# Performance work log

Measured on AMD Instinct MI355X. Metric: run time of the kernel, lower is better.

## Reference

```python
import jax, jax.numpy as jnp
import numpy as np

HID, H, D, DFF = 128, 4, 128, 2048   # hidden_dim, nheads, out_feats per head, dim_feedforward
N, E, B = 32768, 524288, 32
EPS = 1e-5
SLOPE = 0.2  # DGL EdgeGATConv negative_slope default


def setup_inputs() -> dict:
    key = jax.random.key(0)
    ks = jax.random.split(key, 16)
    s = 0.05
    return {
        "h": jax.random.normal(ks[0], (N, HID), jnp.float32),
        "e": jax.random.normal(ks[1], (E, 1), jnp.float32),
        "src": jax.random.randint(ks[2], (E,), 0, N, jnp.int32),
        "dst": jax.random.randint(ks[3], (E,), 0, N, jnp.int32),
        "batch_size": B,
        # EdgeGATConv params (fc / fc_edge / res_fc are bias-free in DGL)
        "W_fc": jax.random.normal(ks[4], (HID, H * D), jnp.float32) * s,
        "attn_l": jax.random.normal(ks[5], (H, D), jnp.float32) * s,
        "attn_r": jax.random.normal(ks[6], (H, D), jnp.float32) * s,
        "W_fe": jax.random.normal(ks[7], (1, H * D), jnp.float32) * s,
        "attn_e": jax.random.normal(ks[8], (H, D), jnp.float32) * s,
        "W_res": jax.random.normal(ks[9], (HID, H * D), jnp.float32) * s,
        "gat_bias": jnp.zeros((H * D,), jnp.float32),
        # linear_mha + norms + FFN
        "W_mha": jax.random.normal(ks[10], (H * D, HID), jnp.float32) * s,
        "b_mha": jnp.zeros((HID,), jnp.float32),
        "n1_g": jnp.ones((HID,), jnp.float32),
        "n1_b": jnp.zeros((HID,), jnp.float32),
        "n2_g": jnp.ones((HID,), jnp.float32),
        "n2_b": jnp.zeros((HID,), jnp.float32),
        "W1": jax.random.normal(ks[11], (HID, DFF), jnp.float32) * s,
        "b1": jnp.zeros((DFF,), jnp.float32),
        "W2": jax.random.normal(ks[12], (DFF, HID), jnp.float32) * s,
        "b2": jnp.zeros((HID,), jnp.float32),
    }


def _ln(x, g, b):
    mu = x.mean(-1, keepdims=True)
    var = ((x - mu) ** 2).mean(-1, keepdims=True)
    return (x - mu) * jax.lax.rsqrt(var + EPS) * g + b


def reference(h, e, src, dst, batch_size, W_fc, attn_l, attn_r, W_fe, attn_e,
              W_res, gat_bias, W_mha, b_mha, n1_g, n1_b, n2_g, n2_b,
              W1, b1, W2, b2):
    n = h.shape[0]
    h0 = h
    # --- EdgeGATConv (eval mode: dropouts are identity) ---
    ft = (h @ W_fc).reshape(n, H, D)                         # (N,H,D)
    el = jnp.einsum("nhd,hd->nh", ft, attn_l)                # (N,H)
    er = jnp.einsum("nhd,hd->nh", ft, attn_r)
    fe = (e @ W_fe).reshape(-1, H, D)                        # (E,H,D)
    ee = jnp.einsum("ehd,hd->eh", fe, attn_e)                # (E,H)
    sc = jax.nn.leaky_relu(el[src] + er[dst] + ee, SLOPE)    # (E,H)
    # segment softmax over incoming edges of each dst node
    m = jax.ops.segment_max(sc, dst, num_segments=n)         # (N,H)
    m = jnp.where(jnp.isfinite(m), m, 0.0)                   # empty segments
    w = jnp.exp(sc - m[dst])
    z = jax.ops.segment_sum(w, dst, num_segments=n)
    zd = z[dst]
    alpha = w / jnp.where(zd == 0, 1.0, zd)                  # (E,H)
    msg = ft[src] * alpha[:, :, None]                        # (E,H,D)
    rst = jax.ops.segment_sum(msg, dst, num_segments=n)      # (N,H,D)
    rst = rst + (h0 @ W_res).reshape(n, H, D) + gat_bias.reshape(1, H, D)
    # --- transformer wrapper ---
    x = jax.nn.relu(rst).reshape(n, H * D)
    x = jax.nn.relu(x @ W_mha + b_mha)
    x = _ln(h0 + x, n1_g, n1_b)
    x = x.reshape(batch_size, -1, x.shape[1])                # (B, N/B, HID)
    ff = jax.nn.relu(x @ W1 + b1) @ W2 + b2
    return _ln(x + ff, n2_g, n2_b)
```

## Files before the change

### kernel.cpp

```cpp
#include <hip/hip_runtime.h>
#include <hip/hip_bf16.h>

#define N_NODES 32768
#define E_EDGES 524288
#define HIDDIM 128
#define FDIM 512
#define DFF 2048
#define LN_EPS 1e-5f
#define SLOPE 0.2f
#define CAP 64

typedef __bf16 bf16_t;
typedef __bf16 bf16x8 __attribute__((ext_vector_type(8)));
typedef float f32x4 __attribute__((ext_vector_type(4)));
typedef float f32x2 __attribute__((ext_vector_type(2)));

#define GLD_LDS16(gp, lp) __builtin_amdgcn_global_load_lds( \
    (const __attribute__((address_space(1))) unsigned int*)(gp), \
    (__attribute__((address_space(3))) unsigned int*)(lp), 16, 0, 0)

__device__ inline unsigned char f32_to_e4m3(float v) {
#if __has_builtin(__builtin_amdgcn_cvt_pk_fp8_f32)
    return (unsigned char)(__builtin_amdgcn_cvt_pk_fp8_f32(v, v, 0, false) & 0xff);
#else
    unsigned bits = __float_as_uint(v);
    unsigned sign = (bits >> 24) & 0x80;
    float av = fabsf(v);
    if (av >= 448.f) return (unsigned char)(sign | 0x7E);
    int e = (int)((bits >> 23) & 0xFF) - 127;
    if (e < -6) { int n = (int)rintf(av * 512.f); return (unsigned char)(sign | n); }
    float ulp = exp2f((float)(e - 3));
    int n = (int)rintf(av / ulp);
    if (n == 16) { e += 1; n = 8; }
    return (unsigned char)(sign | ((e + 7) << 3) | (n - 8));
#endif
}
template<bool HI>
__device__ inline f32x2 e4m3x2_to_f32(unsigned u) {
#if __has_builtin(__builtin_amdgcn_cvt_pk_f32_fp8)
    return __builtin_amdgcn_cvt_pk_f32_fp8(u, HI);
#else
    f32x2 r;
    unsigned b0 = HI ? ((u >> 16) & 0xff) : (u & 0xff);
    unsigned b1 = HI ? ((u >> 24) & 0xff) : ((u >> 8) & 0xff);
    unsigned bs[2] = {b0, b1};
    for (int i = 0; i < 2; ++i) {
        unsigned b = bs[i];
        float s = (b & 0x80) ? -1.f : 1.f;
        int e = (b >> 3) & 15, m = b & 7;
        float v = e ? (8 + m) * exp2f((float)(e - 10)) : m * exp2f(-9.f);
        r[i] = s * v;
    }
    return r;
#endif
}

__device__ inline void pack_range(const float* __restrict__ B, bf16_t* __restrict__ out,
                                  int id, int N) {
    const int g = id / N, n = id % N;
    union { bf16_t b[8]; uint4 u; } pk;
#pragma unroll
    for (int j = 0; j < 8; ++j) pk.b[j] = (bf16_t)B[(size_t)(g * 8 + j) * N + n];
    *(uint4*)(out + (size_t)id * 8) = pk.u;
}

__global__ __launch_bounds__(256) void prep_kernel(const float* __restrict__ h, bf16_t* __restrict__ hb,
                                                   const float* __restrict__ W_fc, bf16_t* __restrict__ Wfc_p,
                                                   const float* __restrict__ W_res, bf16_t* __restrict__ Wres_p,
                                                   const float* __restrict__ W_mha, bf16_t* __restrict__ Wmha_p,
                                                   const float* __restrict__ W1, bf16_t* __restrict__ W1_p,
                                                   const float* __restrict__ W2, bf16_t* __restrict__ W2_p,
                                                   const float* __restrict__ W_fe, const float* __restrict__ attn_e,
                                                   float* __restrict__ ce) {
    int bid = blockIdx.x;
    const int tid = threadIdx.x;
    if (bid < 4096) {
        const int id = bid * 256 + tid;
        const float4 v = ((const float4*)h)[id];
        union { bf16_t b[4]; uint2 u; } pk;
        pk.b[0] = (bf16_t)v.x; pk.b[1] = (bf16_t)v.y; pk.b[2] = (bf16_t)v.z; pk.b[3] = (bf16_t)v.w;
        *(uint2*)(hb + (size_t)id * 4) = pk.u;
        return;
    }
    bid -= 4096;
    if (bid < 32)  { pack_range(W_fc,  Wfc_p,  bid * 256 + tid, 512);  return; }
    bid -= 32;
    if (bid < 32)  { pack_range(W_res, Wres_p, bid * 256 + tid, 512);  return; }
    bid -= 32;
    if (bid < 32)  { pack_range(W_mha, Wmha_p, bid * 256 + tid, 128);  return; }
    bid -= 32;
    if (bid < 128) { pack_range(W1,    W1_p,   bid * 256 + tid, 2048); return; }
    bid -= 128;
    if (bid < 128) { pack_range(W2,    W2_p,   bid * 256 + tid, 128);  return; }
    if (tid < 128) {
        const float4 w = ((const float4*)W_fe)[tid];
        const float4 a = ((const float4*)attn_e)[tid];
        float p = w.x * a.x + w.y * a.y + w.z * a.z + w.w * a.w;
        for (int off = 16; off; off >>= 1) p += __shfl_down(p, off, 32);
        if ((tid & 31) == 0) ce[tid >> 5] = p;
    }
}

__global__ __launch_bounds__(256) void gemm_mfma(const bf16_t* __restrict__ A,
                                                 const bf16_t* __restrict__ Bp,
                                                 bf16_t* __restrict__ C,
                                                 int M, int N, int K) {
    __shared__ __align__(16) bf16_t lA[4096];
    __shared__ __align__(16) bf16_t lB[4096];
    const int tid = threadIdx.x;
    const int lane = tid & 63;
    const int wave = tid >> 6;
    const int wm = (wave >> 1) * 64, wn = (wave & 1) * 64;
    const int row0 = blockIdx.y * 128, col0 = blockIdx.x * 128;
    const int ko = lane >> 4;
    const int rl = lane & 15;
    f32x4 acc[4][4] = {};
    const int c0 = tid, c1 = tid + 256;
    const int g0 = c0 >> 7, m0 = c0 & 127;
    const int g1 = c1 >> 7, m1 = c1 & 127;
    for (int k0 = 0; k0 < K; k0 += 32) {
        __syncthreads();
        GLD_LDS16(A + (size_t)(row0 + m0) * K + k0 + g0 * 8, lA + c0 * 8);
        GLD_LDS16(A + (size_t)(row0 + m1) * K + k0 + g1 * 8, lA + c1 * 8);
        GLD_LDS16(Bp + ((size_t)(k0 / 8 + g0) * N + col0 + m0) * 8, lB + c0 * 8);
        GLD_LDS16(Bp + ((size_t)(k0 / 8 + g1) * N + col0 + m1) * 8, lB + c1 * 8);
        __syncthreads();
        bf16x8 af[4], bfr[4];
#pragma unroll
        for (int i = 0; i < 4; ++i) {
            af[i]  = *(const bf16x8*)&lA[(ko * 128 + wm + i * 16 + rl) * 8];
            bfr[i] = *(const bf16x8*)&lB[(ko * 128 + wn + i * 16 + rl) * 8];
        }
#pragma unroll
        for (int i = 0; i < 4; ++i)
#pragma unroll
            for (int j = 0; j < 4; ++j)
                acc[i][j] = __builtin_amdgcn_mfma_f32_16x16x32_bf16(af[i], bfr[j], acc[i][j], 0, 0, 0);
    }
    const int cr = (lane >> 4) * 4;
    const int cc = lane & 15;
#pragma unroll
    for (int i = 0; i < 4; ++i)
#pragma unroll
        for (int j = 0; j < 4; ++j) {
            const int col = col0 + wn + j * 16 + cc;
#pragma unroll
            for (int r = 0; r < 4; ++r) {
                const int row = row0 + wm + i * 16 + cr + r;
                C[(size_t)row * N + col] = (bf16_t)acc[i][j][r];
            }
        }
}

__global__ __launch_bounds__(256) void gemm_ft(const bf16_t* __restrict__ A,
                                               const bf16_t* __restrict__ Bp,
                                               const float* __restrict__ attn_l,
                                               const float* __restrict__ attn_r,
                                               unsigned char* __restrict__ ft8,
                                               float* __restrict__ el,
                                               float* __restrict__ er) {
    __shared__ __align__(16) bf16_t lA[4096];
    __shared__ __align__(16) bf16_t lB[4096];
    __shared__ float s_el[2][128], s_er[2][128];
    const int tid = threadIdx.x, lane = tid & 63, wave = tid >> 6;
    const int wm = (wave >> 1) * 64, wn = (wave & 1) * 64;
    const int row0 = blockIdx.y * 128;
    const int head = blockIdx.x, col0 = head * 128;
    const int ko = lane >> 4, rl = lane & 15;
    f32x4 acc[4][4] = {};
    const int c0 = tid, c1 = tid + 256;
    const int g0 = c0 >> 7, m0 = c0 & 127;
    const int g1 = c1 >> 7, m1 = c1 & 127;
    for (int k0 = 0; k0 < 128; k0 += 32) {
        __syncthreads();
        GLD_LDS16(A + (size_t)(row0 + m0) * 128 + k0 + g0 * 8, lA + c0 * 8);
        GLD_LDS16(A + (size_t)(row0 + m1) * 128 + k0 + g1 * 8, lA + c1 * 8);
        GLD_LDS16(Bp + ((size_t)(k0 / 8 + g0) * 512 + col0 + m0) * 8, lB + c0 * 8);
        GLD_LDS16(Bp + ((size_t)(k0 / 8 + g1) * 512 + col0 + m1) * 8, lB + c1 * 8);
        __syncthreads();
        bf16x8 af[4], bfr[4];
#pragma unroll
        for (int i = 0; i < 4; ++i) {
            af[i]  = *(const bf16x8*)&lA[(ko * 128 + wm + i * 16 + rl) * 8];
            bfr[i] = *(const bf16x8*)&lB[(ko * 128 + wn + i * 16 + rl) * 8];
        }
#pragma unroll
        for (int i = 0; i < 4; ++i)
#pragma unroll
            for (int j = 0; j < 4; ++j)
                acc[i][j] = __builtin_amdgcn_mfma_f32_16x16x32_bf16(af[i], bfr[j], acc[i][j], 0, 0, 0);
    }
    const int cr = (lane >> 4) * 4, cc = lane & 15;
    float al[4], ar[4];
#pragma unroll
    for (int j = 0; j < 4; ++j) {
        al[j] = attn_l[col0 + wn + j * 16 + cc];
        ar[j] = attn_r[col0 + wn + j * 16 + cc];
    }
#pragma unroll
    for (int i = 0; i < 4; ++i)
#pragma unroll
        for (int r = 0; r < 4; ++r) {
            const int row = row0 + wm + i * 16 + cr + r;
            float pel = 0.f, per = 0.f;
#pragma unroll
            for (int j = 0; j < 4; ++j) {
                const float v = acc[i][j][r];
                ft8[(size_t)row * 512 + col0 + wn + j * 16 + cc] = f32_to_e4m3(v);
                pel += v * al[j];
                per += v * ar[j];
            }
#pragma unroll
            for (int m = 1; m < 16; m <<= 1) {
                pel += __shfl_xor(pel, m);
                per += __shfl_xor(per, m);
            }
            if (cc == 0) {
                s_el[wn >> 6][wm + i * 16 + cr + r] = pel;
                s_er[wn >> 6][wm + i * 16 + cr + r] = per;
            }
        }
    __syncthreads();
    if (tid < 128) {
        el[(size_t)(row0 + tid) * 4 + head] = s_el[0][tid] + s_el[1][tid];
        er[(size_t)(row0 + tid) * 4 + head] = s_er[0][tid] + s_er[1][tid];
    }
}

__global__ __launch_bounds__(256) void gemm_mha_ln(const bf16_t* __restrict__ A,
                                                   const bf16_t* __restrict__ Bp,
                                                   const float* __restrict__ bias,
                                                   const float* __restrict__ h0,
                                                   const float* __restrict__ gamma,
                                                   const float* __restrict__ beta,
                                                   bf16_t* __restrict__ out) {
    __shared__ __align__(16) bf16_t lA[4096];
    __shared__ __align__(16) bf16_t lB[4096];
    __shared__ float s_s1[2][128], s_s2[2][128], s_mu[128], s_rs[128];
    const int tid = threadIdx.x, lane = tid & 63, wave = tid >> 6;
    const int wm = (wave >> 1) * 64, wn = (wave & 1) * 64;
    const int row0 = blockIdx.x * 128;
    const int ko = lane >> 4, rl = lane & 15;
    f32x4 acc[4][4] = {};
    const int c0 = tid, c1 = tid + 256;
    const int g0 = c0 >> 7, m0 = c0 & 127;
    const int g1 = c1 >> 7, m1 = c1 & 127;
    for (int k0 = 0; k0 < 512; k0 += 32) {
        __syncthreads();
        GLD_LDS16(A + (size_t)(row0 + m0) * 512 + k0 + g0 * 8, lA + c0 * 8);
        GLD_LDS16(A + (size_t)(row0 + m1) * 512 + k0 + g1 * 8, lA + c1 * 8);
        GLD_LDS16(Bp + ((size_t)(k0 / 8 + g0) * 128 + m0) * 8, lB + c0 * 8);
        GLD_LDS16(Bp + ((size_t)(k0 / 8 + g1) * 128 + m1) * 8, lB + c1 * 8);
        __syncthreads();
        bf16x8 af[4], bfr[4];
#pragma unroll
        for (int i = 0; i < 4; ++i) {
            af[i]  = *(const bf16x8*)&lA[(ko * 128 + wm + i * 16 + rl) * 8];
            bfr[i] = *(const bf16x8*)&lB[(ko * 128 + wn + i * 16 + rl) * 8];
        }
#pragma unroll
        for (int i = 0; i < 4; ++i)
#pragma unroll
            for (int j = 0; j < 4; ++j)
                acc[i][j] = __builtin_amdgcn_mfma_f32_16x16x32_bf16(af[i], bfr[j], acc[i][j], 0, 0, 0);
    }
    const int cr = (lane >> 4) * 4, cc = lane & 15;
#pragma unroll
    for (int j = 0; j < 4; ++j) {
        const int col = wn + j * 16 + cc;
        const float bb = bias[col];
#pragma unroll
        for (int i = 0; i < 4; ++i)
#pragma unroll
            for (int r = 0; r < 4; ++r) {
                const int row = row0 + wm + i * 16 + cr + r;
                acc[i][j][r] = fmaxf(acc[i][j][r] + bb, 0.f) + h0[(size_t)row * 128 + col];
            }
    }
#pragma unroll
    for (int i = 0; i < 4; ++i)
#pragma unroll
        for (int r = 0; r < 4; ++r) {
            float s1 = 0.f, s2 = 0.f;
#pragma unroll
            for (int j = 0; j < 4; ++j) { const float v = acc[i][j][r]; s1 += v; s2 += v * v; }
#pragma unroll
            for (int m = 1; m < 16; m <<= 1) {
                s1 += __shfl_xor(s1, m);
                s2 += __shfl_xor(s2, m);
            }
            if (cc == 0) {
                s_s1[wn >> 6][wm + i * 16 + cr + r] = s1;
                s_s2[wn >> 6][wm + i * 16 + cr + r] = s2;
            }
        }
    __syncthreads();
    if (tid < 128) {
        const float a = s_s1[0][tid] + s_s1[1][tid];
        const float q = s_s2[0][tid] + s_s2[1][tid];
        const float mu = a * (1.f / 128.f);
        s_mu[tid] = mu;
        s_rs[tid] = rsqrtf(q * (1.f / 128.f) - mu * mu + LN_EPS);
    }
    __syncthreads();
#pragma unroll
    for (int j = 0; j < 4; ++j) {
        const int col = wn + j * 16 + cc;
        const float gg = gamma[col], bb = beta[col];
#pragma unroll
        for (int i = 0; i < 4; ++i)
#pragma unroll
            for (int r = 0; r < 4; ++r) {
                const int rloc = wm + i * 16 + cr + r;
                out[(size_t)(row0 + rloc) * 128 + col] =
                    (bf16_t)((acc[i][j][r] - s_mu[rloc]) * s_rs[rloc] * gg + bb);
            }
    }
}

__global__ __launch_bounds__(256, 2) void ffn_fused(const bf16_t* __restrict__ x3,
                                                    const bf16_t* __restrict__ W1p,
                                                    const float* __restrict__ b1,
                                                    const bf16_t* __restrict__ W2p,
                                                    const float* __restrict__ b2,
                                                    const float* __restrict__ gamma,
                                                    const float* __restrict__ beta,
                                                    float* __restrict__ out) {
    __shared__ __align__(16) bf16_t lW1[8192];
    __shared__ __align__(16) bf16_t lW2[8192];
    __shared__ __align__(16) bf16_t lY[4096];
    __shared__ float s_s1[2][64], s_s2[2][64], s_mu[64], s_rs[64];
    const int tid = threadIdx.x, lane = tid & 63, wave = tid >> 6;
    const int wr  = (wave >> 1) * 32;
    const int wc1 = (wave & 1) * 32;
    const int wc2 = (wave & 1) * 64;
    const int row0 = blockIdx.x * 64;
    const int ko = lane >> 4, rl = lane & 15;
    const int cr = ko * 4, cc = rl;

#pragma unroll
    for (int it = 0; it < 4; ++it) {
        const int c = it * 256 + tid, g = c >> 6, m = c & 63;
        GLD_LDS16(x3 + (size_t)(row0 + m) * 128 + g * 8, lW1 + c * 8);
    }
    __syncthreads();
    bf16x8 afx[2][4];
#pragma unroll
    for (int i = 0; i < 2; ++i)
#pragma unroll
        for (int kk = 0; kk < 4; ++kk)
            afx[i][kk] = *(const bf16x8*)&lW1[((kk * 4 + ko) * 64 + wr + i * 16 + rl) * 8];

    f32x4 xacc[2][4] = {};
    for (int ch = 0; ch < 32; ++ch) {
        __syncthreads();
#pragma unroll
        for (int it = 0; it < 4; ++it) {
            const int c = it * 256 + tid;
            { const int g = c >> 6, n = c & 63;  GLD_LDS16(W1p + ((size_t)g * 2048 + ch * 64 + n) * 8, lW1 + c * 8); }
            { const int g = c >> 7, n = c & 127; GLD_LDS16(W2p + ((size_t)(ch * 8 + g) * 128 + n) * 8, lW2 + c * 8); }
        }
        __syncthreads();
        f32x4 yacc[2][2] = {};
#pragma unroll
        for (int kk = 0; kk < 4; ++kk) {
            bf16x8 bfr[2];
#pragma unroll
            for (int j = 0; j < 2; ++j)
                bfr[j] = *(const bf16x8*)&lW1[((kk * 4 + ko) * 64 + wc1 + j * 16 + rl) * 8];
#pragma unroll
            for (int i = 0; i < 2; ++i)
#pragma unroll
                for (int j = 0; j < 2; ++j)
                    yacc[i][j] = __builtin_amdgcn_mfma_f32_16x16x32_bf16(afx[i][kk], bfr[j], yacc[i][j], 0, 0, 0);
        }
#pragma unroll
        for (int j = 0; j < 2; ++j) {
            const int dff = wc1 + j * 16 + cc;
            const float bb = b1[ch * 64 + dff];
#pragma unroll
            for (int i = 0; i < 2; ++i)
#pragma unroll
                for (int r = 0; r < 4; ++r)
                    lY[((dff >> 3) * 64 + wr + i * 16 + cr + r) * 8 + (dff & 7)] =
                        (bf16_t)fmaxf(yacc[i][j][r] + bb, 0.f);
        }
        __syncthreads();
#pragma unroll
        for (int kk = 0; kk < 2; ++kk) {
            bf16x8 afY[2], bfr2[4];
#pragma unroll
            for (int i = 0; i < 2; ++i)
                afY[i] = *(const bf16x8*)&lY[((kk * 4 + ko) * 64 + wr + i * 16 + rl) * 8];
#pragma unroll
            for (int j = 0; j < 4; ++j)
                bfr2[j] = *(const bf16x8*)&lW2[((kk * 4 + ko) * 128 + wc2 + j * 16 + rl) * 8];
#pragma unroll
            for (int i = 0; i < 2; ++i)
#pragma unroll
                for (int j = 0; j < 4; ++j)
                    xacc[i][j] = __builtin_amdgcn_mfma_f32_16x16x32_bf16(afY[i], bfr2[j], xacc[i][j], 0, 0, 0);
        }
    }
#pragma unroll
    for (int j = 0; j < 4; ++j) {
        const int col = wc2 + j * 16 + cc;
        const float bb = b2[col];
#pragma unroll
        for (int i = 0; i < 2; ++i)
#pragma unroll
            for (int r = 0; r < 4; ++r) {
                const int row = wr + i * 16 + cr + r;
                xacc[i][j][r] += bb + (float)x3[(size_t)(row0 + row) * 128 + col];
            }
    }
#pragma unroll
    for (int i = 0; i < 2; ++i)
#pragma unroll
        for (int r = 0; r < 4; ++r) {
            float s1 = 0.f, s2 = 0.f;
#pragma unroll
            for (int j = 0; j < 4; ++j) { const float v = xacc[i][j][r]; s1 += v; s2 += v * v; }
#pragma unroll
            for (int m = 1; m < 16; m <<= 1) {
                s1 += __shfl_xor(s1, m);
                s2 += __shfl_xor(s2, m);
            }
            if (cc == 0) {
                s_s1[wave & 1][wr + i * 16 + cr + r] = s1;
                s_s2[wave & 1][wr + i * 16 + cr + r] = s2;
            }
        }
    __syncthreads();
    if (tid < 64) {
        const float a = s_s1[0][tid] + s_s1[1][tid];
        const float q = s_s2[0][tid] + s_s2[1][tid];
        const float mu = a * (1.f / 128.f);
        s_mu[tid] = mu;
        s_rs[tid] = rsqrtf(q * (1.f / 128.f) - mu * mu + LN_EPS);
    }
    __syncthreads();
#pragma unroll
    for (int j = 0; j < 4; ++j) {
        const int col = wc2 + j * 16 + cc;
        const float gg = gamma[col], bb = beta[col];
#pragma unroll
        for (int i = 0; i < 2; ++i)
#pragma unroll
            for (int r = 0; r < 4; ++r) {
                const int rloc = wr + i * 16 + cr + r;
                out[(size_t)(row0 + rloc) * 128 + col] =
                    (xacc[i][j][r] - s_mu[rloc]) * s_rs[rloc] * gg + bb;
            }
    }
}

__global__ __launch_bounds__(256) void edge_build(const float* __restrict__ evals,
                                                  const int* __restrict__ src,
                                                  const int* __restrict__ dst,
                                                  const float* __restrict__ el,
                                                  const float* __restrict__ er,
                                                  const float* __restrict__ ce,
                                                  int* __restrict__ cursor,
                                                  int* __restrict__ csr_src,
                                                  float4* __restrict__ csr_w) {
    const int e = blockIdx.x * 256 + threadIdx.x;
    const int s = src[e], d = dst[e];
    const float ev = evals[e];
    const float4 l = *(const float4*)(el + (size_t)s * 4);
    const float4 r = *(const float4*)(er + (size_t)d * 4);
    const float4 c = *(const float4*)ce;
    float4 w;
    {
        float v;
        v = l.x + r.x + ev * c.x; v = v >= 0.f ? v : SLOPE * v; w.x = __expf(v);
        v = l.y + r.y + ev * c.y; v = v >= 0.f ? v : SLOPE * v; w.y = __expf(v);
        v = l.z + r.z + ev * c.z; v = v >= 0.f ? v : SLOPE * v; w.z = __expf(v);
        v = l.w + r.w + ev * c.w; v = v >= 0.f ? v : SLOPE * v; w.w = __expf(v);
    }
    const int pos = atomicAdd(&cursor[d], 1);
    if (pos < CAP) {
        csr_src[(size_t)d * CAP + pos] = s;
        csr_w[(size_t)d * CAP + pos] = w;
    }
}

__global__ __launch_bounds__(128) void aggregate_kernel(const unsigned char* __restrict__ ft8,
                                                        const bf16_t* __restrict__ res,
                                                        const int* __restrict__ cursor,
                                                        const int* __restrict__ csr_src,
                                                        const float4* __restrict__ csr_w,
                                                        const float* __restrict__ gat_bias,
                                                        bf16_t* __restrict__ x1) {
    const int n = blockIdx.x, t = threadIdx.x;
    __shared__ int s_src[CAP];
    __shared__ float s_w[CAP][4];
    const int deg = min(cursor[n], CAP);
    const int ht = t >> 5;
    if (t < deg) {
        s_src[t] = csr_src[(size_t)n * CAP + t];
        *(float4*)s_w[t] = csr_w[(size_t)n * CAP + t];
    }
    __syncthreads();
    float4 acc = {0.f, 0.f, 0.f, 0.f};
    float z = 0.f;
    for (int j = 0; j < deg; ++j) {
        const float w = s_w[j][ht];
        z += w;
        const unsigned u = *(const unsigned*)(ft8 + (size_t)s_src[j] * 512 + t * 4);
        const f32x2 lo = e4m3x2_to_f32<false>(u);
        const f32x2 hi = e4m3x2_to_f32<true>(u);
        acc.x += w * lo[0]; acc.y += w * lo[1];
        acc.z += w * hi[0]; acc.w += w * hi[1];
    }
    const float rz = deg > 0 ? 1.f / z : 0.f;
    const uint2 ur = *(const uint2*)(res + (size_t)n * FDIM + t * 4);
    const float4 gb = ((const float4*)gat_bias)[t];
    union { bf16_t b[4]; uint2 u; } pk;
    pk.b[0] = (bf16_t)fmaxf(acc.x * rz + __uint_as_float(ur.x << 16) + gb.x, 0.f);
    pk.b[1] = (bf16_t)fmaxf(acc.y * rz + __uint_as_float(ur.x & 0xFFFF0000u) + gb.y, 0.f);
    pk.b[2] = (bf16_t)fmaxf(acc.z * rz + __uint_as_float(ur.y << 16) + gb.z, 0.f);
    pk.b[3] = (bf16_t)fmaxf(acc.w * rz + __uint_as_float(ur.y & 0xFFFF0000u) + gb.w, 0.f);
    *(uint2*)(x1 + (size_t)n * FDIM + t * 4) = pk.u;
}

extern "C" void kernel_launch(void* const* d_in, const int* in_sizes, int n_in,
                              void* d_out, int out_size, void* d_ws, size_t ws_size,
                              hipStream_t stream) {
    const float* h        = (const float*)d_in[0];
    const float* evals    = (const float*)d_in[1];
    const int*   src      = (const int*)d_in[2];
    const int*   dst      = (const int*)d_in[3];
    const float* W_fc     = (const float*)d_in[5];
    const float* attn_l   = (const float*)d_in[6];
    const float* attn_r   = (const float*)d_in[7];
    const float* W_fe     = (const float*)d_in[8];
    const float* attn_e   = (const float*)d_in[9];
    const float* W_res    = (const float*)d_in[10];
    const float* gat_bias = (const float*)d_in[11];
    const float* W_mha    = (const float*)d_in[12];
    const float* b_mha    = (const float*)d_in[13];
    const float* n1_g     = (const float*)d_in[14];
    const float* n1_b     = (const float*)d_in[15];
    const float* n2_g     = (const float*)d_in[16];
    const float* n2_b     = (const float*)d_in[17];
    const float* W1       = (const float*)d_in[18];
    const float* b1       = (const float*)d_in[19];
    const float* W2       = (const float*)d_in[20];
    const float* b2       = (const float*)d_in[21];

    char* ws = (char*)d_ws;
    unsigned char* ft8 = (unsigned char*)(ws + 0);
    bf16_t* res     = (bf16_t*)(ws + 16777216ull);
    bf16_t* x1      = (bf16_t*)(ws + 50331648ull);
    float4* csr_w   = (float4*)(ws + 83886080ull);
    int*    csr_src = (int*)   (ws + 117440512ull);
    bf16_t* x3b     = (bf16_t*)(ws + 125829120ull);
    bf16_t* hb      = (bf16_t*)(ws + 134217728ull);
    bf16_t* Wfc_p   = (bf16_t*)(ws + 142606336ull);
    bf16_t* Wres_p  = (bf16_t*)(ws + 142737408ull);
    bf16_t* Wmha_p  = (bf16_t*)(ws + 142868480ull);
    bf16_t* W1_p    = (bf16_t*)(ws + 142999552ull);
    bf16_t* W2_p    = (bf16_t*)(ws + 143523840ull);
    float*  el      = (float*) (ws + 144048128ull);
    float*  er      = (float*) (ws + 144572416ull);
    float*  ce      = (float*) (ws + 145096704ull);
    int*    cursor  = (int*)   (ws + 145096768ull);

    if (ws_size < 146000000ull) return;

    (void)hipMemsetAsync(cursor, 0, 131072, stream);

    prep_kernel<<<4449, 256, 0, stream>>>(h, hb, W_fc, Wfc_p, W_res, Wres_p,
                                          W_mha, Wmha_p, W1, W1_p, W2, W2_p,
                                          W_fe, attn_e, ce);
    gemm_ft<<<dim3(4, 256), 256, 0, stream>>>(hb, Wfc_p, attn_l, attn_r, ft8, el, er);
    gemm_mfma<<<dim3(4, 256), 256, 0, stream>>>(hb, Wres_p, res, N_NODES, FDIM, 128);
    edge_build<<<E_EDGES / 256, 256, 0, stream>>>(evals, src, dst, el, er, ce, cursor, csr_src, csr_w);
    aggregate_kernel<<<N_NODES, 128, 0, stream>>>(ft8, res, cursor, csr_src, csr_w, gat_bias, x1);
    gemm_mha_ln<<<256, 256, 0, stream>>>(x1, Wmha_p, b_mha, h, n1_g, n1_b, x3b);
    ffn_fused<<<512, 256, 0, stream>>>(x3b, W1_p, b1, W2_p, b2, n2_g, n2_b, (float*)d_out);
}
```

Before: 297.7 us.

## Merge ft/res GEMMs into one launch and double-buffer FFN weight tiles

The W_fc and W_res weights are packed into one concatenated 1024-column matrix, so a single GEMM launch of 8x256 blocks produces both the fp8 ft/el/er outputs and the bf16 residual. This removes one kernel launch and a second pass over the node features. Separately, the fused FFN kernel now double-buffers its W1/W2 chunks in LDS, prefetching the next chunk while computing the current one. Each wave also owns 16 full rows, so the LayerNorm reduction stays within the wave and the shared-memory sync rounds go away. In exchange, LDS use doubles and each wave carries more accumulator registers, which may lower occupancy.

```diff
diff --git a/kernel.cpp b/kernel.cpp
--- a/kernel.cpp
+++ b/kernel.cpp
@@ -63,10 +63,18 @@
     for (int j = 0; j < 8; ++j) pk.b[j] = (bf16_t)B[(size_t)(g * 8 + j) * N + n];
     *(uint4*)(out + (size_t)id * 8) = pk.u;
 }
+__device__ inline void pack_cat(const float* __restrict__ B, bf16_t* __restrict__ out,
+                                int id, int base) {
+    const int g = id / 512, n = id % 512;
+    union { bf16_t b[8]; uint4 u; } pk;
+#pragma unroll
+    for (int j = 0; j < 8; ++j) pk.b[j] = (bf16_t)B[(size_t)(g * 8 + j) * 512 + n];
+    *(uint4*)(out + ((size_t)g * 1024 + base + n) * 8) = pk.u;
+}
 
 __global__ __launch_bounds__(256) void prep_kernel(const float* __restrict__ h, bf16_t* __restrict__ hb,
-                                                   const float* __restrict__ W_fc, bf16_t* __restrict__ Wfc_p,
-                                                   const float* __restrict__ W_res, bf16_t* __restrict__ Wres_p,
+                                                   const float* __restrict__ W_fc,
+                                                   const float* __restrict__ W_res, bf16_t* __restrict__ Wcat_p,
                                                    const float* __restrict__ W_mha, bf16_t* __restrict__ Wmha_p,
                                                    const float* __restrict__ W1, bf16_t* __restrict__ W1_p,
                                                    const float* __restrict__ W2, bf16_t* __restrict__ W2_p,
@@ -83,9 +91,9 @@
         return;
     }
     bid -= 4096;
-    if (bid < 32)  { pack_range(W_fc,  Wfc_p,  bid * 256 + tid, 512);  return; }
+    if (bid < 32)  { pack_cat(W_fc,  Wcat_p, bid * 256 + tid, 0);    return; }
     bid -= 32;
-    if (bid < 32)  { pack_range(W_res, Wres_p, bid * 256 + tid, 512);  return; }
+    if (bid < 32)  { pack_cat(W_res, Wcat_p, bid * 256 + tid, 512);  return; }
     bid -= 32;
     if (bid < 32)  { pack_range(W_mha, Wmha_p, bid * 256 + tid, 128);  return; }
     bid -= 32;
@@ -101,71 +109,21 @@
     }
 }
 
-__global__ __launch_bounds__(256) void gemm_mfma(const bf16_t* __restrict__ A,
-                                                 const bf16_t* __restrict__ Bp,
-                                                 bf16_t* __restrict__ C,
-                                                 int M, int N, int K) {
-    __shared__ __align__(16) bf16_t lA[4096];
-    __shared__ __align__(16) bf16_t lB[4096];
-    const int tid = threadIdx.x;
-    const int lane = tid & 63;
-    const int wave = tid >> 6;
-    const int wm = (wave >> 1) * 64, wn = (wave & 1) * 64;
-    const int row0 = blockIdx.y * 128, col0 = blockIdx.x * 128;
-    const int ko = lane >> 4;
-    const int rl = lane & 15;
-    f32x4 acc[4][4] = {};
-    const int c0 = tid, c1 = tid + 256;
-    const int g0 = c0 >> 7, m0 = c0 & 127;
-    const int g1 = c1 >> 7, m1 = c1 & 127;
-    for (int k0 = 0; k0 < K; k0 += 32) {
-        __syncthreads();
-        GLD_LDS16(A + (size_t)(row0 + m0) * K + k0 + g0 * 8, lA + c0 * 8);
-        GLD_LDS16(A + (size_t)(row0 + m1) * K + k0 + g1 * 8, lA + c1 * 8);
-        GLD_LDS16(Bp + ((size_t)(k0 / 8 + g0) * N + col0 + m0) * 8, lB + c0 * 8);
-        GLD_LDS16(Bp + ((size_t)(k0 / 8 + g1) * N + col0 + m1) * 8, lB + c1 * 8);
-        __syncthreads();
-        bf16x8 af[4], bfr[4];
-#pragma unroll
-        for (int i = 0; i < 4; ++i) {
-            af[i]  = *(const bf16x8*)&lA[(ko * 128 + wm + i * 16 + rl) * 8];
-            bfr[i] = *(const bf16x8*)&lB[(ko * 128 + wn + i * 16 + rl) * 8];
-        }
-#pragma unroll
-        for (int i = 0; i < 4; ++i)
-#pragma unroll
-            for (int j = 0; j < 4; ++j)
-                acc[i][j] = __builtin_amdgcn_mfma_f32_16x16x32_bf16(af[i], bfr[j], acc[i][j], 0, 0, 0);
-    }
-    const int cr = (lane >> 4) * 4;
-    const int cc = lane & 15;
-#pragma unroll
-    for (int i = 0; i < 4; ++i)
-#pragma unroll
-        for (int j = 0; j < 4; ++j) {
-            const int col = col0 + wn + j * 16 + cc;
-#pragma unroll
-            for (int r = 0; r < 4; ++r) {
-                const int row = row0 + wm + i * 16 + cr + r;
-                C[(size_t)row * N + col] = (bf16_t)acc[i][j][r];
-            }
-        }
-}
-
-__global__ __launch_bounds__(256) void gemm_ft(const bf16_t* __restrict__ A,
-                                               const bf16_t* __restrict__ Bp,
-                                               const float* __restrict__ attn_l,
-                                               const float* __restrict__ attn_r,
-                                               unsigned char* __restrict__ ft8,
-                                               float* __restrict__ el,
-                                               float* __restrict__ er) {
+__global__ __launch_bounds__(256) void gemm_ftres(const bf16_t* __restrict__ A,
+                                                  const bf16_t* __restrict__ Bp,
+                                                  const float* __restrict__ attn_l,
+                                                  const float* __restrict__ attn_r,
+                                                  unsigned char* __restrict__ ft8,
+                                                  bf16_t* __restrict__ res,
+                                                  float* __restrict__ el,
+                                                  float* __restrict__ er) {
     __shared__ __align__(16) bf16_t lA[4096];
     __shared__ __align__(16) bf16_t lB[4096];
     __shared__ float s_el[2][128], s_er[2][128];
     const int tid = threadIdx.x, lane = tid & 63, wave = tid >> 6;
     const int wm = (wave >> 1) * 64, wn = (wave & 1) * 64;
     const int row0 = blockIdx.y * 128;
-    const int head = blockIdx.x, col0 = head * 128;
+    const int col0 = blockIdx.x * 128;
     const int ko = lane >> 4, rl = lane & 15;
     f32x4 acc[4][4] = {};
     const int c0 = tid, c1 = tid + 256;
@@ -175,8 +133,8 @@
         __syncthreads();
         GLD_LDS16(A + (size_t)(row0 + m0) * 128 + k0 + g0 * 8, lA + c0 * 8);
         GLD_LDS16(A + (size_t)(row0 + m1) * 128 + k0 + g1 * 8, lA + c1 * 8);
-        GLD_LDS16(Bp + ((size_t)(k0 / 8 + g0) * 512 + col0 + m0) * 8, lB + c0 * 8);
-        GLD_LDS16(Bp + ((size_t)(k0 / 8 + g1) * 512 + col0 + m1) * 8, lB + c1 * 8);
+        GLD_LDS16(Bp + ((size_t)(k0 / 8 + g0) * 1024 + col0 + m0) * 8, lB + c0 * 8);
+        GLD_LDS16(Bp + ((size_t)(k0 / 8 + g1) * 1024 + col0 + m1) * 8, lB + c1 * 8);
         __syncthreads();
         bf16x8 af[4], bfr[4];
 #pragma unroll
@@ -191,39 +149,55 @@
                 acc[i][j] = __builtin_amdgcn_mfma_f32_16x16x32_bf16(af[i], bfr[j], acc[i][j], 0, 0, 0);
     }
     const int cr = (lane >> 4) * 4, cc = lane & 15;
-    float al[4], ar[4];
-#pragma unroll
-    for (int j = 0; j < 4; ++j) {
-        al[j] = attn_l[col0 + wn + j * 16 + cc];
-        ar[j] = attn_r[col0 + wn + j * 16 + cc];
-    }
-#pragma unroll
-    for (int i = 0; i < 4; ++i)
-#pragma unroll
-        for (int r = 0; r < 4; ++r) {
-            const int row = row0 + wm + i * 16 + cr + r;
-            float pel = 0.f, per = 0.f;
+    if (col0 < 512) {
+        float al[4], ar[4];
+#pragma unroll
+        for (int j = 0; j < 4; ++j) {
+            al[j] = attn_l[col0 + wn + j * 16 + cc];
+            ar[j] = attn_r[col0 + wn + j * 16 + cc];
+        }
+#pragma unroll
+        for (int i = 0; i < 4; ++i)
+#pragma unroll
+            for (int r = 0; r < 4; ++r) {
+                const int row = row0 + wm + i * 16 + cr + r;
+                float pel = 0.f, per = 0.f;
+#pragma unroll
+                for (int j = 0; j < 4; ++j) {
+                    const float v = acc[i][j][r];
+                    ft8[(size_t)row * 512 + col0 + wn + j * 16 + cc] = f32_to_e4m3(v);
+                    pel += v * al[j];
+                    per += v * ar[j];
+                }
+#pragma unroll
+                for (int m = 1; m < 16; m <<= 1) {
+                    pel += __shfl_xor(pel, m);
+                    per += __shfl_xor(per, m);
+                }
+                if (cc == 0) {
+                    s_el[wn >> 6][wm + i * 16 + cr + r] = pel;
+                    s_er[wn >> 6][wm + i * 16 + cr + r] = per;
+                }
+            }
+        __syncthreads();
+        if (tid < 128) {
+            const int head = col0 >> 7;
+            el[(size_t)(row0 + tid) * 4 + head] = s_el[0][tid] + s_el[1][tid];
+            er[(size_t)(row0 + tid) * 4 + head] = s_er[0][tid] + s_er[1][tid];
+        }
+    } else {
+        const int rc0 = col0 - 512;
+#pragma unroll
+        for (int i = 0; i < 4; ++i)
 #pragma unroll
             for (int j = 0; j < 4; ++j) {
-                const float v = acc[i][j][r];
-                ft8[(size_t)row * 512 + col0 + wn + j * 16 + cc] = f32_to_e4m3(v);
-                pel += v * al[j];
-                per += v * ar[j];
-            }
-#pragma unroll
-            for (int m = 1; m < 16; m <<= 1) {
-                pel += __shfl_xor(pel, m);
-                per += __shfl_xor(per, m);
-            }
-            if (cc == 0) {
-                s_el[wn >> 6][wm + i * 16 + cr + r] = pel;
-                s_er[wn >> 6][wm + i * 16 + cr + r] = per;
-            }
-        }
-    __syncthreads();
-    if (tid < 128) {
-        el[(size_t)(row0 + tid) * 4 + head] = s_el[0][tid] + s_el[1][tid];
-        er[(size_t)(row0 + tid) * 4 + head] = s_er[0][tid] + s_er[1][tid];
+                const int col = rc0 + wn + j * 16 + cc;
+#pragma unroll
+                for (int r = 0; r < 4; ++r) {
+                    const int row = row0 + wm + i * 16 + cr + r;
+                    res[(size_t)row * 512 + col] = (bf16_t)acc[i][j][r];
+                }
+            }
     }
 }
 
@@ -326,14 +300,11 @@
                                                     const float* __restrict__ gamma,
                                                     const float* __restrict__ beta,
                                                     float* __restrict__ out) {
-    __shared__ __align__(16) bf16_t lW1[8192];
-    __shared__ __align__(16) bf16_t lW2[8192];
+    __shared__ __align__(16) bf16_t lW1[2][8192];
+    __shared__ __align__(16) bf16_t lW2[2][8192];
     __shared__ __align__(16) bf16_t lY[4096];
-    __shared__ float s_s1[2][64], s_s2[2][64], s_mu[64], s_rs[64];
     const int tid = threadIdx.x, lane = tid & 63, wave = tid >> 6;
-    const int wr  = (wave >> 1) * 32;
-    const int wc1 = (wave & 1) * 32;
-    const int wc2 = (wave & 1) * 64;
+    const int wr = wave * 16;
     const int row0 = blockIdx.x * 64;
     const int ko = lane >> 4, rl = lane & 15;
     const int cr = ko * 4, cc = rl;
@@ -341,117 +312,91 @@
 #pragma unroll
     for (int it = 0; it < 4; ++it) {
         const int c = it * 256 + tid, g = c >> 6, m = c & 63;
-        GLD_LDS16(x3 + (size_t)(row0 + m) * 128 + g * 8, lW1 + c * 8);
+        GLD_LDS16(x3 + (size_t)(row0 + m) * 128 + g * 8, lW1[1] + c * 8);
+    }
+#pragma unroll
+    for (int it = 0; it < 4; ++it) {
+        const int c = it * 256 + tid;
+        { const int g = c >> 6, n = c & 63;  GLD_LDS16(W1p + ((size_t)g * 2048 + n) * 8, lW1[0] + c * 8); }
+        { const int g = c >> 7, n = c & 127; GLD_LDS16(W2p + ((size_t)g * 128 + n) * 8, lW2[0] + c * 8); }
     }
     __syncthreads();
-    bf16x8 afx[2][4];
-#pragma unroll
-    for (int i = 0; i < 2; ++i)
-#pragma unroll
-        for (int kk = 0; kk < 4; ++kk)
-            afx[i][kk] = *(const bf16x8*)&lW1[((kk * 4 + ko) * 64 + wr + i * 16 + rl) * 8];
-
-    f32x4 xacc[2][4] = {};
+    bf16x8 afx[4];
+#pragma unroll
+    for (int kk = 0; kk < 4; ++kk)
+        afx[kk] = *(const bf16x8*)&lW1[1][((kk * 4 + ko) * 64 + wr + rl) * 8];
+
+    f32x4 xacc[8] = {};
     for (int ch = 0; ch < 32; ++ch) {
+        const int b = ch & 1;
         __syncthreads();
-#pragma unroll
-        for (int it = 0; it < 4; ++it) {
-            const int c = it * 256 + tid;
-            { const int g = c >> 6, n = c & 63;  GLD_LDS16(W1p + ((size_t)g * 2048 + ch * 64 + n) * 8, lW1 + c * 8); }
-            { const int g = c >> 7, n = c & 127; GLD_LDS16(W2p + ((size_t)(ch * 8 + g) * 128 + n) * 8, lW2 + c * 8); }
-        }
-        __syncthreads();
-        f32x4 yacc[2][2] = {};
+        if (ch + 1 < 32) {
+            const int nb = b ^ 1, nch = ch + 1;
+#pragma unroll
+            for (int it = 0; it < 4; ++it) {
+                const int c = it * 256 + tid;
+                { const int g = c >> 6, n = c & 63;  GLD_LDS16(W1p + ((size_t)g * 2048 + nch * 64 + n) * 8, lW1[nb] + c * 8); }
+                { const int g = c >> 7, n = c & 127; GLD_LDS16(W2p + ((size_t)(nch * 8 + g) * 128 + n) * 8, lW2[nb] + c * 8); }
+            }
+        }
+        f32x4 yacc[4] = {};
 #pragma unroll
         for (int kk = 0; kk < 4; ++kk) {
-            bf16x8 bfr[2];
-#pragma unroll
-            for (int j = 0; j < 2; ++j)
-                bfr[j] = *(const bf16x8*)&lW1[((kk * 4 + ko) * 64 + wc1 + j * 16 + rl) * 8];
-#pragma unroll
-            for (int i = 0; i < 2; ++i)
-#pragma unroll
-                for (int j = 0; j < 2; ++j)
-                    yacc[i][j] = __builtin_amdgcn_mfma_f32_16x16x32_bf16(afx[i][kk], bfr[j], yacc[i][j], 0, 0, 0);
-        }
-#pragma unroll
-        for (int j = 0; j < 2; ++j) {
-            const int dff = wc1 + j * 16 + cc;
+            bf16x8 bfr[4];
+#pragma unroll
+            for (int j = 0; j < 4; ++j)
+                bfr[j] = *(const bf16x8*)&lW1[b][((kk * 4 + ko) * 64 + j * 16 + rl) * 8];
+#pragma unroll
+            for (int j = 0; j < 4; ++j)
+                yacc[j] = __builtin_amdgcn_mfma_f32_16x16x32_bf16(afx[kk], bfr[j], yacc[j], 0, 0, 0);
+        }
+#pragma unroll
+        for (int j = 0; j < 4; ++j) {
+            const int dff = j * 16 + cc;
             const float bb = b1[ch * 64 + dff];
 #pragma unroll
-            for (int i = 0; i < 2; ++i)
-#pragma unroll
-                for (int r = 0; r < 4; ++r)
-                    lY[((dff >> 3) * 64 + wr + i * 16 + cr + r) * 8 + (dff & 7)] =
-                        (bf16_t)fmaxf(yacc[i][j][r] + bb, 0.f);
-        }
-        __syncthreads();
+            for (int r = 0; r < 4; ++r)
+                lY[((dff >> 3) * 64 + wr + cr + r) * 8 + (dff & 7)] =
+                    (bf16_t)fmaxf(yacc[j][r] + bb, 0.f);
+        }
 #pragma unroll
         for (int kk = 0; kk < 2; ++kk) {
-            bf16x8 afY[2], bfr2[4];
-#pragma unroll
-            for (int i = 0; i < 2; ++i)
-                afY[i] = *(const bf16x8*)&lY[((kk * 4 + ko) * 64 + wr + i * 16 + rl) * 8];
-#pragma unroll
-            for (int j = 0; j < 4; ++j)
-                bfr2[j] = *(const bf16x8*)&lW2[((kk * 4 + ko) * 128 + wc2 + j * 16 + rl) * 8];
-#pragma unroll
-            for (int i = 0; i < 2; ++i)
-#pragma unroll
-                for (int j = 0; j < 4; ++j)
-                    xacc[i][j] = __builtin_amdgcn_mfma_f32_16x16x32_bf16(afY[i], bfr2[j], xacc[i][j], 0, 0, 0);
-        }
-    }
-#pragma unroll
-    for (int j = 0; j < 4; ++j) {
-        const int col = wc2 + j * 16 + cc;
+            bf16x8 afY = *(const bf16x8*)&lY[((kk * 4 + ko) * 64 + wr + rl) * 8];
+#pragma unroll
+            for (int j = 0; j < 8; ++j) {
+                bf16x8 bfr2 = *(const bf16x8*)&lW2[b][((kk * 4 + ko) * 128 + j * 16 + rl) * 8];
+                xacc[j] = __builtin_amdgcn_mfma_f32_16x16x32_bf16(afY, bfr2, xacc[j], 0, 0, 0);
+            }
+        }
+    }
+#pragma unroll
+    for (int j = 0; j < 8; ++j) {
+        const int col = j * 16 + cc;
         const float bb = b2[col];
 #pragma unroll
-        for (int i = 0; i < 2; ++i)
-#pragma unroll
-            for (int r = 0; r < 4; ++r) {
-                const int row = wr + i * 16 + cr + r;
-                xacc[i][j][r] += bb + (float)x3[(size_t)(row0 + row) * 128 + col];
-            }
-    }
-#pragma unroll
-    for (int i = 0; i < 2; ++i)
-#pragma unroll
         for (int r = 0; r < 4; ++r) {
-            float s1 = 0.f, s2 = 0.f;
-#pragma unroll
-            for (int j = 0; j < 4; ++j) { const float v = xacc[i][j][r]; s1 += v; s2 += v * v; }
-#pragma unroll
-            for (int m = 1; m < 16; m <<= 1) {
-                s1 += __shfl_xor(s1, m);
-                s2 += __shfl_xor(s2, m);
-            }
-            if (cc == 0) {
-                s_s1[wave & 1][wr + i * 16 + cr + r] = s1;
-                s_s2[wave & 1][wr + i * 16 + cr + r] = s2;
-            }
-        }
-    __syncthreads();
-    if (tid < 64) {
-        const float a = s_s1[0][tid] + s_s1[1][tid];
-        const float q = s_s2[0][tid] + s_s2[1][tid];
-        const float mu = a * (1.f / 128.f);
-        s_mu[tid] = mu;
-        s_rs[tid] = rsqrtf(q * (1.f / 128.f) - mu * mu + LN_EPS);
-    }
-    __syncthreads();
-#pragma unroll
-    for (int j = 0; j < 4; ++j) {
-        const int col = wc2 + j * 16 + cc;
-        const float gg = gamma[col], bb = beta[col];
-#pragma unroll
-        for (int i = 0; i < 2; ++i)
-#pragma unroll
-            for (int r = 0; r < 4; ++r) {
-                const int rloc = wr + i * 16 + cr + r;
-                out[(size_t)(row0 + rloc) * 128 + col] =
-                    (xacc[i][j][r] - s_mu[rloc]) * s_rs[rloc] * gg + bb;
-            }
+            const int row = wr + cr + r;
+            xacc[j][r] += bb + (float)x3[(size_t)(row0 + row) * 128 + col];
+        }
+    }
+#pragma unroll
+    for (int r = 0; r < 4; ++r) {
+        float s1 = 0.f, s2 = 0.f;
+#pragma unroll
+        for (int j = 0; j < 8; ++j) { const float v = xacc[j][r]; s1 += v; s2 += v * v; }
+#pragma unroll
+        for (int m = 1; m < 16; m <<= 1) {
+            s1 += __shfl_xor(s1, m);
+            s2 += __shfl_xor(s2, m);
+        }
+        const float mu = s1 * (1.f / 128.f);
+        const float rs = rsqrtf(s2 * (1.f / 128.f) - mu * mu + LN_EPS);
+        const int row = row0 + wr + cr + r;
+#pragma unroll
+        for (int j = 0; j < 8; ++j) {
+            const int col = j * 16 + cc;
+            out[(size_t)row * 128 + col] = (xacc[j][r] - mu) * rs * gamma[col] + beta[col];
+        }
     }
 }
 
@@ -557,8 +502,7 @@
     int*    csr_src = (int*)   (ws + 117440512ull);
     bf16_t* x3b     = (bf16_t*)(ws + 125829120ull);
     bf16_t* hb      = (bf16_t*)(ws + 134217728ull);
-    bf16_t* Wfc_p   = (bf16_t*)(ws + 142606336ull);
-    bf16_t* Wres_p  = (bf16_t*)(ws + 142737408ull);
+    bf16_t* Wcat_p  = (bf16_t*)(ws + 142606336ull);
     bf16_t* Wmha_p  = (bf16_t*)(ws + 142868480ull);
     bf16_t* W1_p    = (bf16_t*)(ws + 142999552ull);
     bf16_t* W2_p    = (bf16_t*)(ws + 143523840ull);
@@ -571,11 +515,10 @@
 
     (void)hipMemsetAsync(cursor, 0, 131072, stream);
 
-    prep_kernel<<<4449, 256, 0, stream>>>(h, hb, W_fc, Wfc_p, W_res, Wres_p,
+    prep_kernel<<<4449, 256, 0, stream>>>(h, hb, W_fc, W_res, Wcat_p,
                                           W_mha, Wmha_p, W1, W1_p, W2, W2_p,
                                           W_fe, attn_e, ce);
-    gemm_ft<<<dim3(4, 256), 256, 0, stream>>>(hb, Wfc_p, attn_l, attn_r, ft8, el, er);
-    gemm_mfma<<<dim3(4, 256), 256, 0, stream>>>(hb, Wres_p, res, N_NODES, FDIM, 128);
+    gemm_ftres<<<dim3(8, 256), 256, 0, stream>>>(hb, Wcat_p, attn_l, attn_r, ft8, res, el, er);
     edge_build<<<E_EDGES / 256, 256, 0, stream>>>(evals, src, dst, el, er, ce, cursor, csr_src, csr_w);
     aggregate_kernel<<<N_NODES, 128, 0, stream>>>(ft8, res, cursor, csr_src, csr_w, gat_bias, x1);
     gemm_mha_ln<<<256, 256, 0, stream>>>(x1, Wmha_p, b_mha, h, n1_g, n1_b, x3b);
```

After: 314.8 us. 5.7% more time.
